# Kernel tuning notes

Measured on AMD Instinct MI355X. Metric: run time of the kernel, lower is better.

## Reference

```python
import jax, jax.numpy as jnp
import numpy as np

N_HEAD = 12
NEG = 1e9


def setup_inputs() -> dict:
    key = jax.random.key(0)
    k1, k2, k3 = jax.random.split(key, 3)
    B, S, D = 1, 4096, 768
    x = jax.random.normal(k1, (B, S, D), dtype=jnp.float32)
    w_attn = jax.random.normal(k2, (D, 3 * D), dtype=jnp.float32) * 0.02
    b_attn = jnp.zeros((3 * D,), dtype=jnp.float32)
    w_proj = jax.random.normal(k3, (D, D), dtype=jnp.float32) * 0.02
    b_proj = jnp.zeros((D,), dtype=jnp.float32)
    return {"x": x, "w_attn": w_attn, "b_attn": b_attn, "w_proj": w_proj, "b_proj": b_proj}


def reference(x, w_attn, b_attn, w_proj, b_proj):
    B, S, D = x.shape
    H = N_HEAD
    hd = D // H
    qkv = x @ w_attn + b_attn  # [B,S,3D]
    q, k, v = jnp.split(qkv, 3, axis=-1)
    # split heads -> [B,H,S,hd]
    q = q.reshape(B, S, H, hd).transpose(0, 2, 1, 3)
    k = k.reshape(B, S, H, hd).transpose(0, 2, 1, 3)
    v = v.reshape(B, S, H, hd).transpose(0, 2, 1, 3)
    w = jnp.einsum('bhqd,bhkd->bhqk', q, k) / jnp.sqrt(jnp.float32(hd))
    mask = jnp.tril(jnp.ones((S, S), dtype=w.dtype))  # causal tril buffer
    w = w * mask - NEG * (1.0 - mask)
    w = jax.nn.softmax(w, axis=-1)
    a = jnp.einsum('bhqk,bhkd->bhqd', w, v)
    a = a.transpose(0, 2, 1, 3).reshape(B, S, D)  # merge heads
    return a @ w_proj + b_proj
```

## Files before the change

### kernel.cpp

```cpp
#include <hip/hip_runtime.h>

typedef __bf16 bf16x8 __attribute__((ext_vector_type(8)));
typedef float f32x4 __attribute__((ext_vector_type(4)));
typedef float f32x16 __attribute__((ext_vector_type(16)));
typedef unsigned short u16;

__device__ inline u16 f2bf(float f) {
  union { float f; unsigned int u; } v; v.f = f;
  unsigned int r = v.u + 0x7fffu + ((v.u >> 16) & 1u);
  return (u16)(r >> 16);
}

__device__ inline void load_lds16(const void* g, void* l) {
  __builtin_amdgcn_global_load_lds((const __attribute__((address_space(1))) unsigned int*)g,
                                   (__attribute__((address_space(3))) unsigned int*)l, 16, 0, 0);
}

__global__ void cvt_bf16(const float* __restrict__ in, u16* __restrict__ out, int n) {
  int i = (blockIdx.x * blockDim.x + threadIdx.x) * 4;
  if (i < n) {
    float4 v = *(const float4*)(in + i);
    ushort4 o;
    o.x = f2bf(v.x); o.y = f2bf(v.y); o.z = f2bf(v.z); o.w = f2bf(v.w);
    *(ushort4*)(out + i) = o;
  }
}

__global__ void transpose_cvt(const float* __restrict__ in, u16* __restrict__ out, int R, int C) {
  __shared__ float tile[32][33];
  int c0 = blockIdx.x * 32, r0 = blockIdx.y * 32;
  int tx = threadIdx.x;
#pragma unroll
  for (int i = threadIdx.y; i < 32; i += 8)
    tile[i][tx] = in[(size_t)(r0 + i) * C + c0 + tx];
  __syncthreads();
#pragma unroll
  for (int i = threadIdx.y; i < 32; i += 8)
    out[(size_t)(c0 + i) * R + r0 + tx] = f2bf(tile[tx][i]);
}

__global__ __launch_bounds__(256) void vtrans(const u16* __restrict__ qkv, u16* __restrict__ vT) {
  const int h = blockIdx.y;
  const int s0 = blockIdx.x * 64;
  const int tid = threadIdx.x;
  __shared__ u16 T[64][72];
  {
    const int key = tid >> 2, dq = (tid & 3) * 16;
    const u16* g = qkv + (size_t)(s0 + key) * 2304 + 1536 + h * 64 + dq;
    *(uint4*)&T[key][dq] = *(const uint4*)g;
    *(uint4*)&T[key][dq + 8] = *(const uint4*)(g + 8);
  }
  __syncthreads();
  {
    const int d = tid >> 2, sq = (tid & 3) * 16;
    u16 tmp[16];
#pragma unroll
    for (int e = 0; e < 16; ++e) tmp[e] = T[sq + e][d];
    u16* o = vT + ((size_t)h * 64 + d) * 4096 + s0 + sq;
    *(uint4*)o = *(uint4*)tmp;
    *(uint4*)(o + 8) = *(uint4*)(tmp + 8);
  }
}

template <int BF16_OUT>
__global__ __launch_bounds__(256) void gemm_bt(const u16* __restrict__ A, const u16* __restrict__ BT,
                                               const float* __restrict__ bias, void* __restrict__ Cv,
                                               int M, int N, int K) {
  __shared__ __align__(16) u16 As[128 * 32];
  __shared__ __align__(16) u16 Bs[128 * 32];
  const int tid = threadIdx.x;
  const int wave = tid >> 6, lane = tid & 63;
  const int g = lane >> 4, lr = lane & 15;
  const int m0 = blockIdx.y * 128, n0 = blockIdx.x * 128;
  const int wr = (wave >> 1) * 64, wc = (wave & 1) * 64;
  f32x4 acc[4][4] = {};

  for (int k0 = 0; k0 < K; k0 += 32) {
    __syncthreads();
#pragma unroll
    for (int j = 0; j < 2; ++j) {
      const int e = tid * 8 + j * 2048;
      const int r = e >> 5, c = e & 31;
      const u16* ga = A + (size_t)(m0 + r) * K + k0 + c;
      const u16* gb = BT + (size_t)(n0 + r) * K + k0 + c;
      load_lds16(ga, (void*)(As + wave * 512 + j * 2048));
      load_lds16(gb, (void*)(Bs + wave * 512 + j * 2048));
    }
    __syncthreads();
    const u16* pa = As + (wr + lr) * 32 + g * 8;
    const u16* pb = Bs + (wc + lr) * 32 + g * 8;
    bf16x8 a[4], b[4];
#pragma unroll
    for (int i = 0; i < 4; ++i) a[i] = *(const bf16x8*)(pa + i * 16 * 32);
#pragma unroll
    for (int j = 0; j < 4; ++j) b[j] = *(const bf16x8*)(pb + j * 16 * 32);
#pragma unroll
    for (int i = 0; i < 4; ++i)
#pragma unroll
      for (int j = 0; j < 4; ++j)
        acc[i][j] = __builtin_amdgcn_mfma_f32_16x16x32_bf16(a[i], b[j], acc[i][j], 0, 0, 0);
  }

#pragma unroll
  for (int i = 0; i < 4; ++i)
#pragma unroll
    for (int j = 0; j < 4; ++j)
#pragma unroll
      for (int r = 0; r < 4; ++r) {
        int row = m0 + wr + i * 16 + g * 4 + r;
        int col = n0 + wc + j * 16 + lr;
        float v = acc[i][j][r] + bias[col];
        if (BF16_OUT)
          ((u16*)Cv)[(size_t)row * N + col] = f2bf(v);
        else
          ((float*)Cv)[(size_t)row * N + col] = v;
      }
}

template <int CH, int DIRECT>
__global__ __launch_bounds__(64) void attn(const u16* __restrict__ qkv, const u16* __restrict__ vT,
                                           u16* __restrict__ pO, float* __restrict__ pml,
                                           u16* __restrict__ aout) {
  __shared__ __align__(16) u16 KV[4][4096];

  const int bid = blockIdx.x;
  const int h = bid % 12;
  int qt, c;
  if (CH == 64) {
    qt = 127 - bid / 12;
    c = 0;
  } else {
    const int u = 319 - bid / 12;
    if (u < 32) { qt = u; c = 0; }
    else if (u < 96) { qt = 32 + ((u - 32) >> 1); c = (u - 32) & 1; }
    else if (u < 192) { qt = 64 + (u - 96) / 3; c = (u - 96) % 3; }
    else { qt = 96 + ((u - 192) >> 2); c = (u - 192) & 3; }
  }
  const int q0 = qt * 32;
  const int nkt = (qt >> 1) + 1;
  const int t0 = c * CH;
  const int tend = min(nkt, t0 + CH);

  const int l = threadIdx.x;
  const int lr = l & 31;
  const int H = l >> 5;
  const int H4 = H * 4, H8 = H * 8;

  const u16* kgb = qkv + 768 + h * 64;
  const u16* vgb = vT + (size_t)h * 64 * 4096;

  const int srow = l >> 3;
  const int sbase = ((l & 7) ^ srow) << 3;
  int kSo[8], vSo[8];
#pragma unroll
  for (int i = 0; i < 8; ++i) {
    const int sc = sbase ^ (i << 3);
    kSo[i] = (8 * i + srow) * 2304 + sc;
    vSo[i] = (8 * i + srow) * 4096 + sc;
  }

  const u16* Rd[2][4];
#pragma unroll
  for (int b2 = 0; b2 < 2; ++b2) {
    const int row = 32 * b2 + lr;
    const int sw = (row ^ (row >> 3)) & 7;
#pragma unroll
    for (int cc = 0; cc < 4; ++cc)
      Rd[b2][cc] = &KV[0][row * 64 + (((2 * cc + H) ^ sw) << 3)];
  }

  bf16x8 qB[4];
  {
    const u16* qp = qkv + (size_t)(q0 + lr) * 2304 + h * 64;
    const float qs = 0.125f * 1.4426950408889634f;
#pragma unroll
    for (int cc = 0; cc < 4; ++cc) {
      bf16x8 raw = *(const bf16x8*)(qp + 16 * cc + H8);
#pragma unroll
      for (int e = 0; e < 8; ++e) qB[cc][e] = (__bf16)((float)raw[e] * qs);
    }
  }

  f32x16 O[2] = {};
  float mst = -__builtin_inff(), lst = 0.f;

#define STAGE(T, BUF)                                                      \
  {                                                                        \
    const size_t kk = (size_t)(T) * 64;                                    \
    _Pragma("unroll") for (int i = 0; i < 8; ++i) {                        \
      load_lds16(kgb + kk * 2304 + kSo[i], &KV[(BUF)][i * 512]);           \
      load_lds16(vgb + kk + vSo[i], &KV[2 + (BUF)][i * 512]);              \
    }                                                                      \
  }

#define BODY(T, BUF)                                                                        \
  {                                                                                         \
    if ((T) + 1 < tend) {                                                                   \
      STAGE((T) + 1, (BUF) ^ 1);                                                            \
      asm volatile("s_waitcnt vmcnt(16)" ::: "memory");                                     \
    } else {                                                                                \
      asm volatile("s_waitcnt vmcnt(0)" ::: "memory");                                      \
    }                                                                                       \
    __builtin_amdgcn_sched_barrier(0);                                                      \
    f32x16 s[2] = {};                                                                       \
    _Pragma("unroll") for (int kb = 0; kb < 2; ++kb)                                        \
      _Pragma("unroll") for (int cc = 0; cc < 4; ++cc) {                                    \
        bf16x8 kf = *(const bf16x8*)(Rd[kb][cc] + (BUF) * 4096);                            \
        s[kb] = __builtin_amdgcn_mfma_f32_32x32x16_bf16(kf, qB[cc], s[kb], 0, 0, 0);        \
      }                                                                                     \
    bf16x8 vf[2][4];                                                                        \
    _Pragma("unroll") for (int da = 0; da < 2; ++da)                                        \
      _Pragma("unroll") for (int cc = 0; cc < 4; ++cc)                                      \
        vf[da][cc] = *(const bf16x8*)(Rd[da][cc] + 8192 + (BUF) * 4096);                    \
    if ((T) == nkt - 1) {                                                                   \
      const int rel = q0 + lr - (T) * 64;                                                   \
      _Pragma("unroll") for (int kb = 0; kb < 2; ++kb)                                      \
        _Pragma("unroll") for (int r = 0; r < 16; ++r)                                      \
          if (32 * kb + (r & 3) + 8 * (r >> 2) + H4 > rel) s[kb][r] = -__builtin_inff();    \
    }                                                                                       \
    float mx = s[0][0];                                                                     \
    _Pragma("unroll") for (int kb = 0; kb < 2; ++kb)                                        \
      _Pragma("unroll") for (int r = 0; r < 16; ++r) mx = fmaxf(mx, s[kb][r]);              \
    mx = fmaxf(mx, __shfl_xor(mx, 32));                                                     \
    if (__any(mx > mst + 12.f)) {                                                           \
      const float mn = fmaxf(mst, mx);                                                      \
      const float alpha = __builtin_amdgcn_exp2f(mst - mn);                                 \
      mst = mn;                                                                             \
      lst *= alpha;                                                                         \
      O[0] *= alpha;                                                                        \
      O[1] *= alpha;                                                                        \
    }                                                                                       \
    float rs = 0.f;                                                                         \
    _Pragma("unroll") for (int kb = 0; kb < 2; ++kb)                                        \
      _Pragma("unroll") for (int r = 0; r < 16; ++r) {                                      \
        const float p = __builtin_amdgcn_exp2f(s[kb][r] - mst);                             \
        s[kb][r] = p;                                                                       \
        rs += p;                                                                            \
      }                                                                                     \
    rs += __shfl_xor(rs, 32);                                                               \
    lst += rs;                                                                              \
    unsigned w[16];                                                                         \
    _Pragma("unroll") for (int kb = 0; kb < 2; ++kb)                                        \
      _Pragma("unroll") for (int j2 = 0; j2 < 4; ++j2) {                                    \
        asm("v_cvt_pk_bf16_f32 %0, %1, %2"                                                  \
            : "=v"(w[kb * 8 + j2 * 2]) : "v"(s[kb][4 * j2]), "v"(s[kb][4 * j2 + 1]));       \
        asm("v_cvt_pk_bf16_f32 %0, %1, %2"                                                  \
            : "=v"(w[kb * 8 + j2 * 2 + 1]) : "v"(s[kb][4 * j2 + 2]), "v"(s[kb][4 * j2 + 3])); \
      }                                                                                     \
    unsigned recv[8];                                                                       \
    _Pragma("unroll") for (int cc = 0; cc < 4; ++cc)                                        \
      _Pragma("unroll") for (int m = 0; m < 2; ++m) {                                       \
        const unsigned send = H ? w[4 * cc + m] : w[4 * cc + 2 + m];                        \
        recv[cc * 2 + m] = (unsigned)__shfl_xor((int)send, 32);                             \
      }                                                                                     \
    _Pragma("unroll") for (int cc = 0; cc < 4; ++cc) {                                      \
      union { unsigned u[4]; bf16x8 v; } Bp;                                                \
      Bp.u[0] = H ? recv[2 * cc] : w[4 * cc];                                               \
      Bp.u[1] = H ? recv[2 * cc + 1] : w[4 * cc + 1];                                       \
      Bp.u[2] = H ? w[4 * cc + 2] : recv[2 * cc];                                           \
      Bp.u[3] = H ? w[4 * cc + 3] : recv[2 * cc + 1];                                       \
      O[0] = __builtin_amdgcn_mfma_f32_32x32x16_bf16(vf[0][cc], Bp.v, O[0], 0, 0, 0);       \
      O[1] = __builtin_amdgcn_mfma_f32_32x32x16_bf16(vf[1][cc], Bp.v, O[1], 0, 0, 0);       \
    }                                                                                       \
  }

  STAGE(t0, 0);
  int t = t0;
  for (; t + 2 <= tend; t += 2) {
    BODY(t, 0);
    BODY(t + 1, 1);
  }
  if (t < tend) BODY(t, 0);
#undef BODY
#undef STAGE

  if (DIRECT) {
    const float inv = 1.0f / lst;
    u16* orow = aout + (size_t)(q0 + lr) * 768 + h * 64;
#pragma unroll
    for (int da = 0; da < 2; ++da)
#pragma unroll
      for (int j2 = 0; j2 < 4; ++j2) {
        ushort4 st;
        st.x = f2bf(O[da][4 * j2 + 0] * inv);
        st.y = f2bf(O[da][4 * j2 + 1] * inv);
        st.z = f2bf(O[da][4 * j2 + 2] * inv);
        st.w = f2bf(O[da][4 * j2 + 3] * inv);
        *(ushort4*)(orow + 32 * da + 8 * j2 + H4) = st;
      }
  } else {
    const int ncmax = (CH == 16) ? 4 : 1;
    const int slot = (h * 128 + qt) * ncmax + c;
    u16* po = pO + (size_t)slot * 2048 + lr * 64;
#pragma unroll
    for (int da = 0; da < 2; ++da)
#pragma unroll
      for (int j2 = 0; j2 < 4; ++j2) {
        ushort4 st;
        st.x = f2bf(O[da][4 * j2 + 0]);
        st.y = f2bf(O[da][4 * j2 + 1]);
        st.z = f2bf(O[da][4 * j2 + 2]);
        st.w = f2bf(O[da][4 * j2 + 3]);
        *(ushort4*)(po + 32 * da + 8 * j2 + H4) = st;
      }
    if (H == 0) {
      float2 ml; ml.x = mst; ml.y = lst;
      *(float2*)(pml + (size_t)slot * 64 + lr * 2) = ml;
    }
  }
}

__global__ __launch_bounds__(64) void combine(const u16* __restrict__ pO, const float* __restrict__ pml,
                                              u16* __restrict__ aout, int ncmax, int CHv) {
  const int bid = blockIdx.x;
  const int h = bid % 12, qt = bid / 12;
  const int nkt = (qt >> 1) + 1;
  const int nc = (nkt + CHv - 1) / CHv;
  const int sb = (h * 128 + qt) * ncmax;
  const int t = threadIdx.x;
  const int row = t & 31, H = t >> 5;

  float m[4], lw[4];
  float M = -__builtin_inff();
#pragma unroll
  for (int c = 0; c < 4; ++c)
    if (c < nc) {
      m[c] = pml[(size_t)(sb + c) * 64 + row * 2];
      M = fmaxf(M, m[c]);
    }
  float L = 0.f;
#pragma unroll
  for (int c = 0; c < 4; ++c)
    if (c < nc) {
      lw[c] = __builtin_amdgcn_exp2f(m[c] - M);
      L += pml[(size_t)(sb + c) * 64 + row * 2 + 1] * lw[c];
    }

  float acc[32] = {};
#pragma unroll
  for (int c = 0; c < 4; ++c)
    if (c < nc) {
      const u16* p = pO + (size_t)(sb + c) * 2048 + row * 64 + 32 * H;
      const float wgt = lw[c];
#pragma unroll
      for (int k = 0; k < 4; ++k) {
        bf16x8 v = *(const bf16x8*)(p + 8 * k);
#pragma unroll
        for (int e = 0; e < 8; ++e) acc[k * 8 + e] += (float)v[e] * wgt;
      }
    }

  const float inv = 1.0f / L;
  u16 ov[32];
#pragma unroll
  for (int d = 0; d < 32; ++d) ov[d] = f2bf(acc[d] * inv);
  u16* dst = aout + (size_t)(qt * 32 + row) * 768 + h * 64 + 32 * H;
#pragma unroll
  for (int k = 0; k < 4; ++k) *(uint4*)(dst + 8 * k) = *(const uint4*)(ov + 8 * k);
}

extern "C" void kernel_launch(void* const* d_in, const int* in_sizes, int n_in,
                              void* d_out, int out_size, void* d_ws, size_t ws_size,
                              hipStream_t stream) {
  const float* x = (const float*)d_in[0];
  const float* w_attn = (const float*)d_in[1];
  const float* b_attn = (const float*)d_in[2];
  const float* w_proj = (const float*)d_in[3];
  const float* b_proj = (const float*)d_in[4];
  float* out = (float*)d_out;

  const int S = 4096, D = 768;
  u16* xb = (u16*)d_ws;
  u16* wTa = xb + (size_t)S * D;
  u16* wTp = wTa + (size_t)3 * D * D;
  u16* qkv = wTp + (size_t)D * D;
  u16* abuf = qkv + (size_t)S * 3 * D;
  u16* vTb = abuf + (size_t)S * D;
  u16* pO = vTb + (size_t)12 * 64 * 4096;

  const size_t base_bytes = (size_t)(3145728 + 1769472 + 589824 + 9437184 + 3145728 + 3145728) * 2;
  const size_t need16 = base_bytes + (size_t)6144 * 2048 * 2 + (size_t)6144 * 64 * 4;
  const size_t need64 = base_bytes + (size_t)1536 * 2048 * 2 + (size_t)1536 * 64 * 4;

  cvt_bf16<<<(S * D) / 1024, 256, 0, stream>>>(x, xb, S * D);
  transpose_cvt<<<dim3((3 * D) / 32, D / 32), dim3(32, 8), 0, stream>>>(w_attn, wTa, D, 3 * D);
  transpose_cvt<<<dim3(D / 32, D / 32), dim3(32, 8), 0, stream>>>(w_proj, wTp, D, D);
  gemm_bt<1><<<dim3((3 * D) / 128, S / 128), 256, 0, stream>>>(xb, wTa, b_attn, qkv, S, 3 * D, D);
  vtrans<<<dim3(S / 64, 12), 256, 0, stream>>>(qkv, vTb);

  if (ws_size >= need16) {
    float* pml = (float*)(pO + (size_t)6144 * 2048);
    attn<16, 0><<<dim3(12 * 320), 64, 0, stream>>>(qkv, vTb, pO, pml, abuf);
    combine<<<dim3(12 * 128), 64, 0, stream>>>(pO, pml, abuf, 4, 16);
  } else if (ws_size >= need64) {
    float* pml = (float*)(pO + (size_t)1536 * 2048);
    attn<64, 0><<<dim3(12 * 128), 64, 0, stream>>>(qkv, vTb, pO, pml, abuf);
    combine<<<dim3(12 * 128), 64, 0, stream>>>(pO, pml, abuf, 1, 64);
  } else {
    attn<64, 1><<<dim3(12 * 128), 64, 0, stream>>>(qkv, vTb, abuf, (float*)abuf, abuf);
  }

  gemm_bt<0><<<dim3(D / 128, S / 128), 256, 0, stream>>>(abuf, wTp, b_proj, out, S, D, D);
}
```

Measured before the change: 167.7 us.

## Share K/V tiles across four waves per block in flash attention

The attention kernel now runs four waves per 256-thread block, each handling a consecutive 32-row query tile, and all four share the K/V tiles staged in LDS. Each wave loads a quarter of every K/V tile, with barriers around each step. This is meant to cut redundant global/L2 traffic for K and V. In exchange, the waves of a block are synchronized to the longest causal range, and masking switches from -inf to a finite large negative so fully masked tiles stay numerically safe. The 64-chunk split fallback path is removed.

```diff
diff --git a/kernel.cpp b/kernel.cpp
--- a/kernel.cpp
+++ b/kernel.cpp
@@ -117,46 +117,51 @@
       }
 }
 
+#define MNEG 30000.0f
 template <int CH, int DIRECT>
-__global__ __launch_bounds__(64) void attn(const u16* __restrict__ qkv, const u16* __restrict__ vT,
-                                           u16* __restrict__ pO, float* __restrict__ pml,
-                                           u16* __restrict__ aout) {
+__global__ __launch_bounds__(256, 3) void attn(const u16* __restrict__ qkv, const u16* __restrict__ vT,
+                                               u16* __restrict__ pO, float* __restrict__ pml,
+                                               u16* __restrict__ aout) {
   __shared__ __align__(16) u16 KV[4][4096];
 
   const int bid = blockIdx.x;
   const int h = bid % 12;
-  int qt, c;
-  if (CH == 64) {
-    qt = 127 - bid / 12;
+  int g, c;
+  if (DIRECT) {
+    g = 31 - bid / 12;
     c = 0;
   } else {
-    const int u = 319 - bid / 12;
-    if (u < 32) { qt = u; c = 0; }
-    else if (u < 96) { qt = 32 + ((u - 32) >> 1); c = (u - 32) & 1; }
-    else if (u < 192) { qt = 64 + (u - 96) / 3; c = (u - 96) % 3; }
-    else { qt = 96 + ((u - 192) >> 2); c = (u - 192) & 3; }
-  }
-  const int q0 = qt * 32;
-  const int nkt = (qt >> 1) + 1;
-  const int t0 = c * CH;
-  const int tend = min(nkt, t0 + CH);
-
-  const int l = threadIdx.x;
+    const int u = 79 - bid / 12;
+    if (u < 8) { g = u; c = 0; }
+    else if (u < 24) { g = 8 + ((u - 8) >> 1); c = (u - 8) & 1; }
+    else if (u < 48) { g = 16 + (u - 24) / 3; c = (u - 24) % 3; }
+    else { g = 24 + ((u - 48) >> 2); c = (u - 48) & 3; }
+  }
+
+  const int tid = threadIdx.x;
+  const int wave = tid >> 6;
+  const int l = tid & 63;
   const int lr = l & 31;
   const int H = l >> 5;
   const int H4 = H * 4, H8 = H * 8;
 
+  const int qt = 4 * g + wave;
+  const int q0 = qt * 32;
+  const int nkt = (qt >> 1) + 1;
+  const int t0 = DIRECT ? 0 : c * CH;
+  const int tend = min(2 * g + 2, t0 + CH);
+
   const u16* kgb = qkv + 768 + h * 64;
   const u16* vgb = vT + (size_t)h * 64 * 4096;
 
   const int srow = l >> 3;
-  const int sbase = ((l & 7) ^ srow) << 3;
-  int kSo[8], vSo[8];
-#pragma unroll
-  for (int i = 0; i < 8; ++i) {
-    const int sc = sbase ^ (i << 3);
-    kSo[i] = (8 * i + srow) * 2304 + sc;
-    vSo[i] = (8 * i + srow) * 4096 + sc;
+  int kSo[2], vSo[2];
+#pragma unroll
+  for (int i = 0; i < 2; ++i) {
+    const int row = 16 * wave + 8 * i + srow;
+    const int sc = ((l & 7) ^ srow ^ (2 * wave + i)) << 3;
+    kSo[i] = row * 2304 + sc;
+    vSo[i] = row * 4096 + sc;
   }
 
   const u16* Rd[2][4];
@@ -182,14 +187,14 @@
   }
 
   f32x16 O[2] = {};
-  float mst = -__builtin_inff(), lst = 0.f;
+  float mst = -MNEG, lst = 0.f;
 
 #define STAGE(T, BUF)                                                      \
   {                                                                        \
     const size_t kk = (size_t)(T) * 64;                                    \
-    _Pragma("unroll") for (int i = 0; i < 8; ++i) {                        \
-      load_lds16(kgb + kk * 2304 + kSo[i], &KV[(BUF)][i * 512]);           \
-      load_lds16(vgb + kk + vSo[i], &KV[2 + (BUF)][i * 512]);              \
+    _Pragma("unroll") for (int i = 0; i < 2; ++i) {                        \
+      load_lds16(kgb + kk * 2304 + kSo[i], &KV[(BUF)][(2 * wave + i) * 512]); \
+      load_lds16(vgb + kk + vSo[i], &KV[2 + (BUF)][(2 * wave + i) * 512]); \
     }                                                                      \
   }
 
@@ -197,10 +202,11 @@
   {                                                                                         \
     if ((T) + 1 < tend) {                                                                   \
       STAGE((T) + 1, (BUF) ^ 1);                                                            \
-      asm volatile("s_waitcnt vmcnt(16)" ::: "memory");                                     \
+      asm volatile("s_waitcnt vmcnt(4)" ::: "memory");                                      \
     } else {                                                                                \
       asm volatile("s_waitcnt vmcnt(0)" ::: "memory");                                      \
     }                                                                                       \
+    __builtin_amdgcn_s_barrier();                                                           \
     __builtin_amdgcn_sched_barrier(0);                                                      \
     f32x16 s[2] = {};                                                                       \
     _Pragma("unroll") for (int kb = 0; kb < 2; ++kb)                                        \
@@ -212,11 +218,11 @@
     _Pragma("unroll") for (int da = 0; da < 2; ++da)                                        \
       _Pragma("unroll") for (int cc = 0; cc < 4; ++cc)                                      \
         vf[da][cc] = *(const bf16x8*)(Rd[da][cc] + 8192 + (BUF) * 4096);                    \
-    if ((T) == nkt - 1) {                                                                   \
+    if ((T) >= nkt - 1) {                                                                   \
       const int rel = q0 + lr - (T) * 64;                                                   \
       _Pragma("unroll") for (int kb = 0; kb < 2; ++kb)                                      \
         _Pragma("unroll") for (int r = 0; r < 16; ++r)                                      \
-          if (32 * kb + (r & 3) + 8 * (r >> 2) + H4 > rel) s[kb][r] = -__builtin_inff();    \
+          if (32 * kb + (r & 3) + 8 * (r >> 2) + H4 > rel) s[kb][r] = -MNEG;                \
     }                                                                                       \
     float mx = s[0][0];                                                                     \
     _Pragma("unroll") for (int kb = 0; kb < 2; ++kb)                                        \
@@ -262,6 +268,7 @@
       O[0] = __builtin_amdgcn_mfma_f32_32x32x16_bf16(vf[0][cc], Bp.v, O[0], 0, 0, 0);       \
       O[1] = __builtin_amdgcn_mfma_f32_32x32x16_bf16(vf[1][cc], Bp.v, O[1], 0, 0, 0);       \
     }                                                                                       \
+    __builtin_amdgcn_s_barrier();                                                           \
   }
 
   STAGE(t0, 0);
@@ -289,8 +296,7 @@
         *(ushort4*)(orow + 32 * da + 8 * j2 + H4) = st;
       }
   } else {
-    const int ncmax = (CH == 16) ? 4 : 1;
-    const int slot = (h * 128 + qt) * ncmax + c;
+    const int slot = (h * 128 + qt) * 4 + c;
     u16* po = pO + (size_t)slot * 2048 + lr * 64;
 #pragma unroll
     for (int da = 0; da < 2; ++da)
@@ -311,12 +317,12 @@
 }
 
 __global__ __launch_bounds__(64) void combine(const u16* __restrict__ pO, const float* __restrict__ pml,
-                                              u16* __restrict__ aout, int ncmax, int CHv) {
+                                              u16* __restrict__ aout, int CHv) {
   const int bid = blockIdx.x;
   const int h = bid % 12, qt = bid / 12;
   const int nkt = (qt >> 1) + 1;
   const int nc = (nkt + CHv - 1) / CHv;
-  const int sb = (h * 128 + qt) * ncmax;
+  const int sb = (h * 128 + qt) * 4;
   const int t = threadIdx.x;
   const int row = t & 31, H = t >> 5;
 
@@ -380,7 +386,6 @@
 
   const size_t base_bytes = (size_t)(3145728 + 1769472 + 589824 + 9437184 + 3145728 + 3145728) * 2;
   const size_t need16 = base_bytes + (size_t)6144 * 2048 * 2 + (size_t)6144 * 64 * 4;
-  const size_t need64 = base_bytes + (size_t)1536 * 2048 * 2 + (size_t)1536 * 64 * 4;
 
   cvt_bf16<<<(S * D) / 1024, 256, 0, stream>>>(x, xb, S * D);
   transpose_cvt<<<dim3((3 * D) / 32, D / 32), dim3(32, 8), 0, stream>>>(w_attn, wTa, D, 3 * D);
@@ -390,14 +395,10 @@
 
   if (ws_size >= need16) {
     float* pml = (float*)(pO + (size_t)6144 * 2048);
-    attn<16, 0><<<dim3(12 * 320), 64, 0, stream>>>(qkv, vTb, pO, pml, abuf);
-    combine<<<dim3(12 * 128), 64, 0, stream>>>(pO, pml, abuf, 4, 16);
-  } else if (ws_size >= need64) {
-    float* pml = (float*)(pO + (size_t)1536 * 2048);
-    attn<64, 0><<<dim3(12 * 128), 64, 0, stream>>>(qkv, vTb, pO, pml, abuf);
-    combine<<<dim3(12 * 128), 64, 0, stream>>>(pO, pml, abuf, 1, 64);
+    attn<16, 0><<<dim3(12 * 80), 256, 0, stream>>>(qkv, vTb, pO, pml, abuf);
+    combine<<<dim3(12 * 128), 64, 0, stream>>>(pO, pml, abuf, 16);
   } else {
-    attn<64, 1><<<dim3(12 * 128), 64, 0, stream>>>(qkv, vTb, abuf, (float*)abuf, abuf);
+    attn<64, 1><<<dim3(12 * 32), 256, 0, stream>>>(qkv, vTb, abuf, (float*)abuf, abuf);
   }
 
   gemm_bt<0><<<dim3(D / 128, S / 128), 256, 0, stream>>>(abuf, wTp, b_proj, out, S, D, D);
```

Result: faster. 143.4 us (-14.5%).
